# Performance work log

Measured on AMD Instinct MI355X. Metric: run time of the kernel, lower is better.

## Reference

```python
import jax, jax.numpy as jnp
import numpy as np

B, H, W, C = 8, 224, 224, 96
WS, SS, NH = 7, 3, 3  # window size, shift size, num heads
HD = C // NH
N = WS * WS
nW = (H // WS) * (W // WS)


def _rel_pos_index():
    coords = np.stack(np.meshgrid(np.arange(WS), np.arange(WS), indexing='ij'))  # (2,WS,WS)
    flat = coords.reshape(2, -1)
    rel = (flat[:, :, None] - flat[:, None, :]).transpose(1, 2, 0)  # (N,N,2)
    rel[:, :, 0] += WS - 1
    rel[:, :, 1] += WS - 1
    rel[:, :, 0] *= 2 * WS - 1
    return jnp.asarray(rel.sum(-1))  # (N,N) int


def _shift_mask():
    img = np.zeros((H, W), np.int32)
    cnt = 0
    sls = (slice(0, -WS), slice(-WS, -SS), slice(-SS, None))
    for hs in sls:
        for ws_ in sls:
            img[hs, ws_] = cnt
            cnt += 1
    m = img.reshape(H // WS, WS, W // WS, WS).transpose(0, 2, 1, 3).reshape(-1, N)  # (nW,N)
    diff = m[:, :, None] - m[:, None, :]
    return jnp.asarray(np.where(diff != 0, -100.0, 0.0).astype(np.float32))  # (nW,N,N)


def setup_inputs() -> dict:
    key = jax.random.key(0)
    ks = jax.random.split(key, 10)
    s = 0.02
    return {
        'x': jax.random.normal(ks[0], (B, H * W, C), jnp.float32),
        'mask': _shift_mask(),
        'norm1_g': jnp.ones((C,), jnp.float32),
        'norm1_b': jnp.zeros((C,), jnp.float32),
        'qkv_w': s * jax.random.normal(ks[1], (3 * C, C), jnp.float32),
        'qkv_b': jnp.zeros((3 * C,), jnp.float32),
        'rpb_table': s * jax.random.normal(ks[2], ((2 * WS - 1) * (2 * WS - 1), NH), jnp.float32),
        'proj_w': s * jax.random.normal(ks[3], (C, C), jnp.float32),
        'proj_b': jnp.zeros((C,), jnp.float32),
        'norm2_g': jnp.ones((C,), jnp.float32),
        'norm2_b': jnp.zeros((C,), jnp.float32),
        'fc1_w': s * jax.random.normal(ks[4], (4 * C, C), jnp.float32),
        'fc1_b': jnp.zeros((4 * C,), jnp.float32),
        'fc2_w': s * jax.random.normal(ks[5], (C, 4 * C), jnp.float32),
        'fc2_b': jnp.zeros((C,), jnp.float32),
    }


def _ln(x, g, b):
    mu = x.mean(-1, keepdims=True)
    var = x.var(-1, keepdims=True)
    return (x - mu) * jax.lax.rsqrt(var + 1e-5) * g + b


def _win_partition(x):  # (B,H,W,C) -> (B*nW, N, C)
    x = x.reshape(B, H // WS, WS, W // WS, WS, C)
    return x.transpose(0, 1, 3, 2, 4, 5).reshape(-1, N, C)


def _win_reverse(w):  # (B*nW, N, C) -> (B,H,W,C)
    w = w.reshape(B, H // WS, W // WS, WS, WS, C)
    return w.transpose(0, 1, 3, 2, 4, 5).reshape(B, H, W, C)


def reference(x, mask, norm1_g, norm1_b, qkv_w, qkv_b, rpb_table, proj_w, proj_b,
              norm2_g, norm2_b, fc1_w, fc1_b, fc2_w, fc2_b):
    rel_idx = _rel_pos_index()  # (N,N) constant
    shortcut = x
    h = _ln(x, norm1_g, norm1_b).reshape(B, H, W, C)
    h = jnp.roll(h, shift=(-SS, -SS), axis=(1, 2))  # cyclic shift
    xw = _win_partition(h)  # (B*nW, N, C)
    B_ = xw.shape[0]
    qkv = (xw @ qkv_w.T + qkv_b).reshape(B_, N, 3, NH, HD).transpose(2, 0, 3, 1, 4)
    q, k, v = qkv[0], qkv[1], qkv[2]  # (B_,NH,N,HD)
    scale = HD ** -0.5
    attn = jnp.einsum('bhid,bhjd->bhij', q * scale, k)  # (B_,NH,N,N)
    bias = rpb_table[rel_idx.reshape(-1)].reshape(N, N, NH).transpose(2, 0, 1)  # (NH,N,N)
    attn = attn + bias[None]
    attn = attn.reshape(B, nW, NH, N, N) + mask[None, :, None]
    attn = jax.nn.softmax(attn.reshape(B_, NH, N, N), axis=-1)
    out = jnp.einsum('bhij,bhjd->bhid', attn, v).transpose(0, 2, 1, 3).reshape(B_, N, C)
    out = out @ proj_w.T + proj_b
    h = _win_reverse(out)
    h = jnp.roll(h, shift=(SS, SS), axis=(1, 2)).reshape(B, H * W, C)
    x = shortcut + h
    # MLP
    m = _ln(x, norm2_g, norm2_b)
    m = jax.nn.gelu(m @ fc1_w.T + fc1_b, approximate=False)
    m = m @ fc2_w.T + fc2_b
    return x + m
```

## Files before the change

kernel.cpp:

```cpp
#include <hip/hip_runtime.h>
#include <hip/hip_bf16.h>
#include <stdint.h>

typedef __attribute__((ext_vector_type(4))) float f32x4;
typedef __bf16 bfv8 __attribute__((ext_vector_type(8)));
typedef unsigned short u16x8 __attribute__((ext_vector_type(8)));
typedef unsigned short u16x4 __attribute__((ext_vector_type(4)));

#define DEV static __device__ __forceinline__

DEV float b2f(unsigned short h) {
    unsigned u = ((unsigned)h) << 16;
    return __builtin_bit_cast(float, u);
}
DEV unsigned short f2b(float f) {
    unsigned u = __builtin_bit_cast(unsigned, f);
    u += 0x7fffu + ((u >> 16) & 1u);
    return (unsigned short)(u >> 16);
}
DEV unsigned short f2bn(float f) {
    return __builtin_bit_cast(unsigned short, (__bf16)f);
}
DEV bfv8 ldb8(const unsigned short* p) {
    return __builtin_bit_cast(bfv8, *(const u16x8*)p);
}
DEV void stb4(unsigned short* p, f32x4 v) {
    u16x4 o;
    o[0] = f2bn(v[0]); o[1] = f2bn(v[1]); o[2] = f2bn(v[2]); o[3] = f2bn(v[3]);
    *(u16x4*)p = o;
}

static constexpr int T = 401408;

__global__ __launch_bounds__(256) void k_prep(const float* __restrict__ qkvw,
                                              const float* __restrict__ projw,
                                              const float* __restrict__ w1,
                                              const float* __restrict__ w2,
                                              const float* __restrict__ rpb,
                                              const float* __restrict__ mask,
                                              unsigned short* __restrict__ wb,
                                              float* __restrict__ cmb) {
    int i = blockIdx.x * 256 + threadIdx.x;
    if (i < 110592) {
        float v;
        if (i < 27648) v = qkvw[i];
        else if (i < 36864) v = projw[i - 27648];
        else if (i < 73728) v = w1[i - 36864];
        else v = w2[i - 73728];
        wb[i] = f2b(v);
    } else if (i < 110592 + 49152) {
        int j = i - 110592;
        int t = j / 12288, rem = j - t * 12288;
        int h = rem >> 12, nm = rem & 4095;
        int n = nm >> 6, m = nm & 63;
        float v = -10000.f;
        if (n < 49 && m < 49) {
            int i1 = n / 7, j1 = n - i1 * 7, i2 = m / 7, j2 = m - i2 * 7;
            int rel = (i1 - i2 + 6) * 13 + (j1 - j2 + 6);
            int rep = ((t & 1) ? 31 : 0) + ((t & 2) ? 992 : 0);
            v = rpb[rel * 3 + h] + mask[rep * 2401 + n * 49 + m];
        }
        cmb[j] = v;
    }
}

__global__ __launch_bounds__(192) void k_attnf(const float* __restrict__ x,
                                               const float* __restrict__ g1,
                                               const float* __restrict__ be1,
                                               const unsigned short* __restrict__ qkvwb,
                                               const float* __restrict__ qkvb,
                                               const float* __restrict__ cmb,
                                               unsigned short* __restrict__ aout) {
    __shared__ unsigned short smem[10368 + 3 * 5120];
    unsigned short* xs = smem;

    unsigned win = blockIdx.x;
    unsigned b = win >> 10, widx = win & 1023u;
    unsigned wi = widx >> 5, wj = widx & 31u;
    int tid = threadIdx.x, wv = tid >> 6, lane = tid & 63;
    int half = lane >> 5, lch = lane & 31;

    for (int it = 0; it < 9; ++it) {
        int tok = it * 6 + wv * 2 + half;
        if (tok < 49) {
            unsigned i = (unsigned)tok / 7u, j = (unsigned)tok - i * 7u;
            unsigned sr = wi * 7 + i + 3; if (sr >= 224) sr -= 224;
            unsigned sc = wj * 7 + j + 3; if (sc >= 224) sc -= 224;
            const float* src = x + (size_t)(b * 50176u + sr * 224u + sc) * 96;
            float v0 = src[lch], v1 = src[lch + 32], v2 = src[lch + 64];
            float s = v0 + v1 + v2, q = v0 * v0 + v1 * v1 + v2 * v2;
#pragma unroll
            for (int off = 1; off < 32; off <<= 1) {
                s += __shfl_xor(s, off);
                q += __shfl_xor(q, off);
            }
            float mu = s * (1.f / 96.f);
            float rstd = rsqrtf(q * (1.f / 96.f) - mu * mu + 1e-5f);
            xs[tok * 104 + lch]      = f2bn((v0 - mu) * rstd * g1[lch] + be1[lch]);
            xs[tok * 104 + lch + 32] = f2bn((v1 - mu) * rstd * g1[lch + 32] + be1[lch + 32]);
            xs[tok * 104 + lch + 64] = f2bn((v2 - mu) * rstd * g1[lch + 64] + be1[lch + 64]);
        }
    }
    for (int t = tid; t < 15 * 96; t += 192)
        xs[(49 + t / 96) * 104 + (t % 96)] = 0;
    __syncthreads();

    int h = wv;
    int rlo = lane & 15, g4 = lane >> 4;
    bfv8 a[4][3];
#pragma unroll
    for (int mt = 0; mt < 4; ++mt)
#pragma unroll
        for (int ks = 0; ks < 3; ++ks)
            a[mt][ks] = ldb8(xs + (mt * 16 + rlo) * 104 + ks * 32 + g4 * 8);
    __syncthreads();

    unsigned short* vtH = smem + h * 3456;
    unsigned short* qH  = smem + 10368 + h * 5120;
    unsigned short* kH  = qH + 2560;
    unsigned short* pH  = qH;

    const float SC = 0.17677669529663687f;
    int colbase[6] = {32 * h, 32 * h + 16, 96 + 32 * h, 96 + 32 * h + 16,
                      192 + 32 * h, 192 + 32 * h + 16};
#pragma unroll
    for (int grp = 0; grp < 2; ++grp) {
        bfv8 wS[3][3];
        f32x4 bS[3];
#pragma unroll
        for (int q3 = 0; q3 < 3; ++q3) {
            int c = colbase[grp * 3 + q3] + rlo;
            wS[q3][0] = ldb8(qkvwb + (size_t)c * 96 + g4 * 8);
            wS[q3][1] = ldb8(qkvwb + (size_t)c * 96 + 32 + g4 * 8);
            wS[q3][2] = ldb8(qkvwb + (size_t)c * 96 + 64 + g4 * 8);
            bS[q3] = *(const f32x4*)(qkvb + colbase[grp * 3 + q3] + g4 * 4);
        }
#pragma unroll
        for (int q3 = 0; q3 < 3; ++q3) {
            int nt = grp * 3 + q3;
#pragma unroll
            for (int mt = 0; mt < 4; ++mt) {
                f32x4 acc = {0.f, 0.f, 0.f, 0.f};
                acc = __builtin_amdgcn_mfma_f32_16x16x32_bf16(wS[q3][0], a[mt][0], acc, 0, 0, 0);
                acc = __builtin_amdgcn_mfma_f32_16x16x32_bf16(wS[q3][1], a[mt][1], acc, 0, 0, 0);
                acc = __builtin_amdgcn_mfma_f32_16x16x32_bf16(wS[q3][2], a[mt][2], acc, 0, 0, 0);
                int token = mt * 16 + rlo;
                if (nt < 2) {
                    f32x4 v = (acc + bS[q3]) * SC;
                    stb4(qH + token * 40 + nt * 16 + g4 * 4, v);
                } else if (nt < 4) {
                    f32x4 v = acc + bS[q3];
                    stb4(kH + token * 40 + (nt - 2) * 16 + g4 * 4, v);
                } else {
#pragma unroll
                    for (int r = 0; r < 4; ++r)
                        vtH[((nt - 4) * 16 + g4 * 4 + r) * 72 + token] =
                            f2bn(acc[r] + bS[q3][r]);
                }
            }
        }
    }
    vtH[32 * 72 + lane] = 0x3F80;

    bfv8 qf[4], kf[4];
#pragma unroll
    for (int t = 0; t < 4; ++t) {
        qf[t] = ldb8(qH + (t * 16 + rlo) * 40 + g4 * 8);
        kf[t] = ldb8(kH + (t * 16 + rlo) * 40 + g4 * 8);
    }
    f32x4 s[4][4];
#pragma unroll
    for (int mt = 0; mt < 4; ++mt)
#pragma unroll
        for (int nt = 0; nt < 4; ++nt) {
            f32x4 acc0 = {0.f, 0.f, 0.f, 0.f};
            s[mt][nt] = __builtin_amdgcn_mfma_f32_16x16x32_bf16(kf[nt], qf[mt], acc0, 0, 0, 0);
        }
    int type = ((wi == 31) ? 2 : 0) | ((wj == 31) ? 1 : 0);
    const float* crow = cmb + ((size_t)(type * 3 + h) << 12);
#pragma unroll
    for (int mt = 0; mt < 4; ++mt) {
        int query = mt * 16 + rlo;
        const float* cr = crow + query * 64;
#pragma unroll
        for (int nt = 0; nt < 4; ++nt) {
            f32x4 cv = *(const f32x4*)(cr + nt * 16 + g4 * 4);
            f32x4 p;
#pragma unroll
            for (int r = 0; r < 4; ++r) p[r] = __expf(s[mt][nt][r] + cv[r]);
            stb4(pH + query * 72 + nt * 16 + g4 * 4, p);
        }
    }
    bfv8 vf[2][3];
#pragma unroll
    for (int ks = 0; ks < 2; ++ks)
#pragma unroll
        for (int db = 0; db < 3; ++db)
            vf[ks][db] = ldb8(vtH + (db * 16 + rlo) * 72 + ks * 32 + g4 * 8);
#pragma unroll
    for (int mt = 0; mt < 4; ++mt) {
        bfv8 pa0 = ldb8(pH + (mt * 16 + rlo) * 72 + g4 * 8);
        bfv8 pa1 = ldb8(pH + (mt * 16 + rlo) * 72 + 32 + g4 * 8);
        f32x4 acc[3];
#pragma unroll
        for (int db = 0; db < 3; ++db) {
            acc[db] = {0.f, 0.f, 0.f, 0.f};
            acc[db] = __builtin_amdgcn_mfma_f32_16x16x32_bf16(vf[0][db], pa0, acc[db], 0, 0, 0);
            acc[db] = __builtin_amdgcn_mfma_f32_16x16x32_bf16(vf[1][db], pa1, acc[db], 0, 0, 0);
        }
        float inv = 1.f / __shfl(acc[2][0], rlo);
        int query = mt * 16 + rlo;
        if (query < 49) {
            unsigned short* ob = aout + ((size_t)win * 49 + query) * 96 + h * 32;
#pragma unroll
            for (int db = 0; db < 2; ++db) {
                f32x4 v = acc[db] * inv;
                stb4(ob + db * 16 + g4 * 4, v);
            }
        }
    }
}

__global__ __launch_bounds__(256, 3) void k_pm(const unsigned short* __restrict__ aout,
                                               const unsigned short* __restrict__ projwb,
                                               const float* __restrict__ projb,
                                               const float* __restrict__ x,
                                               const float* __restrict__ g2,
                                               const float* __restrict__ be2,
                                               const unsigned short* __restrict__ w1b,
                                               const float* __restrict__ bias1,
                                               const unsigned short* __restrict__ w2b,
                                               const float* __restrict__ bias2,
                                               float* __restrict__ out) {
    __shared__ unsigned short smem[64 * 204];
    unsigned short* xn  = smem;
    unsigned short* m1t = smem;

    int lane = threadIdx.x & 63, wv = threadIdx.x >> 6;
    int rlo = lane & 15, g4 = lane >> 4;
    size_t tok0 = (size_t)blockIdx.x * 64;
    size_t rowW = tok0 + wv * 16;

    bfv8 a0[3];
    {
        const unsigned short* p = aout + (rowW + rlo) * 96 + g4 * 8;
        a0[0] = ldb8(p); a0[1] = ldb8(p + 32); a0[2] = ldb8(p + 64);
    }
    int pix;
    {
        unsigned wt = (unsigned)(rowW + rlo);
        unsigned win = wt / 49u, n = wt - win * 49u;
        unsigned b = win >> 10, widx = win & 1023u;
        unsigned wi = widx >> 5, wj = widx & 31u;
        unsigned i = n / 7u, j = n - i * 7u;
        unsigned sr = wi * 7 + i + 3; if (sr >= 224) sr -= 224;
        unsigned sc = wj * 7 + j + 3; if (sc >= 224) sc -= 224;
        pix = (int)(b * 50176u + sr * 224u + sc);
    }
    f32x4 xr4[6];
#pragma unroll
    for (int nt = 0; nt < 6; ++nt)
        xr4[nt] = *(const f32x4*)(x + (size_t)pix * 96 + nt * 16 + g4 * 4);

    f32x4 xv[6];
    float rs = 0.f, rq = 0.f;
    for (int nt = 0; nt < 6; ++nt) {
        int c = nt * 16 + rlo;
        bfv8 b0 = ldb8(projwb + (size_t)c * 96 + g4 * 8);
        bfv8 b1 = ldb8(projwb + (size_t)c * 96 + 32 + g4 * 8);
        bfv8 b2 = ldb8(projwb + (size_t)c * 96 + 64 + g4 * 8);
        f32x4 bv = *(const f32x4*)(projb + nt * 16 + g4 * 4);
        f32x4 acc = {0.f, 0.f, 0.f, 0.f};
        acc = __builtin_amdgcn_mfma_f32_16x16x32_bf16(b0, a0[0], acc, 0, 0, 0);
        acc = __builtin_amdgcn_mfma_f32_16x16x32_bf16(b1, a0[1], acc, 0, 0, 0);
        acc = __builtin_amdgcn_mfma_f32_16x16x32_bf16(b2, a0[2], acc, 0, 0, 0);
        f32x4 v = acc + bv + xr4[nt];
        xv[nt] = v;
#pragma unroll
        for (int r = 0; r < 4; ++r) {
            rs += v[r];
            rq += v[r] * v[r];
        }
    }
    rs += __shfl_xor(rs, 16); rq += __shfl_xor(rq, 16);
    rs += __shfl_xor(rs, 32); rq += __shfl_xor(rq, 32);
    float mu = rs * (1.f / 96.f);
    float rstd = rsqrtf(rq * (1.f / 96.f) - mu * mu + 1e-5f);
#pragma unroll
    for (int nt = 0; nt < 6; ++nt) {
        f32x4 gg = *(const f32x4*)(g2 + nt * 16 + g4 * 4);
        f32x4 bb = *(const f32x4*)(be2 + nt * 16 + g4 * 4);
        f32x4 v;
#pragma unroll
        for (int r = 0; r < 4; ++r) v[r] = (xv[nt][r] - mu) * rstd * gg[r] + bb[r];
        stb4(xn + (wv * 16 + rlo) * 104 + nt * 16 + g4 * 4, v);
    }
    __syncthreads();

    bfv8 a[4][3];
#pragma unroll
    for (int mt = 0; mt < 4; ++mt)
#pragma unroll
        for (int ks = 0; ks < 3; ++ks)
            a[mt][ks] = ldb8(xn + (mt * 16 + rlo) * 104 + ks * 32 + g4 * 8);
    __syncthreads();

    f32x4 acc2[6];
#pragma unroll
    for (int nt = 0; nt < 6; ++nt) acc2[nt] = {0.f, 0.f, 0.f, 0.f};

#pragma unroll
    for (int half = 0; half < 2; ++half) {
#pragma unroll
        for (int nt = 0; nt < 3; ++nt) {
            int cb = half * 192 + wv * 48 + nt * 16;
            int c = cb + rlo;
            bfv8 b0 = ldb8(w1b + (size_t)c * 96 + g4 * 8);
            bfv8 b1 = ldb8(w1b + (size_t)c * 96 + 32 + g4 * 8);
            bfv8 b2 = ldb8(w1b + (size_t)c * 96 + 64 + g4 * 8);
            f32x4 bv = *(const f32x4*)(bias1 + cb + g4 * 4);
#pragma unroll
            for (int mt = 0; mt < 4; ++mt) {
                f32x4 acc = {0.f, 0.f, 0.f, 0.f};
                acc = __builtin_amdgcn_mfma_f32_16x16x32_bf16(b0, a[mt][0], acc, 0, 0, 0);
                acc = __builtin_amdgcn_mfma_f32_16x16x32_bf16(b1, a[mt][1], acc, 0, 0, 0);
                acc = __builtin_amdgcn_mfma_f32_16x16x32_bf16(b2, a[mt][2], acc, 0, 0, 0);
                f32x4 g;
#pragma unroll
                for (int r = 0; r < 4; ++r) {
                    float v = acc[r] + bv[r];
                    float z = 1.5957691216057308f * (v + 0.044715f * v * v * v);
                    g[r] = v / (1.f + __expf(-z));
                }
                stb4(m1t + (mt * 16 + rlo) * 204 + wv * 48 + nt * 16 + g4 * 4, g);
            }
        }
        __syncthreads();
#pragma unroll
        for (int ks = 0; ks < 6; ++ks) {
            bfv8 am = ldb8(m1t + (wv * 16 + rlo) * 204 + ks * 32 + g4 * 8);
#pragma unroll
            for (int nt = 0; nt < 6; ++nt) {
                bfv8 bw = ldb8(w2b + (size_t)(nt * 16 + rlo) * 384 + half * 192 + ks * 32 + g4 * 8);
                acc2[nt] = __builtin_amdgcn_mfma_f32_16x16x32_bf16(bw, am, acc2[nt], 0, 0, 0);
            }
        }
        if (half == 0) __syncthreads();
    }

#pragma unroll
    for (int nt = 0; nt < 6; ++nt) {
        f32x4 bv = *(const f32x4*)(bias2 + nt * 16 + g4 * 4);
        f32x4 ov = acc2[nt] + bv + xv[nt];
        *(f32x4*)(out + (size_t)pix * 96 + nt * 16 + g4 * 4) = ov;
    }
}

extern "C" void kernel_launch(void* const* d_in, const int* in_sizes, int n_in,
                              void* d_out, int out_size, void* d_ws, size_t ws_size,
                              hipStream_t stream) {
    const float* x     = (const float*)d_in[0];
    const float* mask  = (const float*)d_in[1];
    const float* n1g   = (const float*)d_in[2];
    const float* n1b   = (const float*)d_in[3];
    const float* qkvw  = (const float*)d_in[4];
    const float* qkvb  = (const float*)d_in[5];
    const float* rpb   = (const float*)d_in[6];
    const float* projw = (const float*)d_in[7];
    const float* projb = (const float*)d_in[8];
    const float* n2g   = (const float*)d_in[9];
    const float* n2b   = (const float*)d_in[10];
    const float* fc1w  = (const float*)d_in[11];
    const float* fc1b  = (const float*)d_in[12];
    const float* fc2w  = (const float*)d_in[13];
    const float* fc2b  = (const float*)d_in[14];

    if (ws_size < 77488128ULL) return;
    char* ws = (char*)d_ws;
    unsigned short* aout = (unsigned short*)ws;
    unsigned short* wb   = (unsigned short*)(ws + 77070336);
    float*          cmb  = (float*)(ws + 77291520);
    float*          out  = (float*)d_out;

    unsigned short* qkvwb  = wb;
    unsigned short* projwb = wb + 27648;
    unsigned short* fc1wb  = wb + 36864;
    unsigned short* fc2wb  = wb + 73728;

    k_prep<<<624, 256, 0, stream>>>(qkvw, projw, fc1w, fc2w, rpb, mask, wb, cmb);
    k_attnf<<<8192, 192, 0, stream>>>(x, n1g, n1b, qkvwb, qkvb, cmb, aout);
    k_pm<<<T / 64, 256, 0, stream>>>(aout, projwb, projb, x, n2g, n2b,
                                     fc1wb, fc1b, fc2wb, fc2b, out);
}
```

Baseline: 520.4 us.

## Rewrite MLP kernel as single-wave tiles using register shuffles instead of LDS

The proj+MLP kernel changes from 4-wave blocks of 64 tokens sharing LDS to 1-wave blocks of 16 tokens. The LayerNorm output and the GELU hidden activations are moved from the MFMA accumulator layout into the operand layout with cross-lane shuffles, so no shared memory and no __syncthreads are needed. The cost is that each wave now loads the full fc1/fc2 weights for only 16 tokens instead of sharing them across 64, which quadruples weight traffic through L1/L2. It also adds shuffle instructions in the inner loop.

```diff
diff --git a/kernel.cpp b/kernel.cpp
--- a/kernel.cpp
+++ b/kernel.cpp
@@ -6,6 +6,7 @@
 typedef __bf16 bfv8 __attribute__((ext_vector_type(8)));
 typedef unsigned short u16x8 __attribute__((ext_vector_type(8)));
 typedef unsigned short u16x4 __attribute__((ext_vector_type(4)));
+typedef unsigned int u32x4 __attribute__((ext_vector_type(4)));
 
 #define DEV static __device__ __forceinline__
 
@@ -28,6 +29,25 @@
     u16x4 o;
     o[0] = f2bn(v[0]); o[1] = f2bn(v[1]); o[2] = f2bn(v[2]); o[3] = f2bn(v[3]);
     *(u16x4*)p = o;
+}
+DEV uint2 pk4(f32x4 v) {
+    uint2 r;
+    r.x = (unsigned)f2bn(v[0]) | ((unsigned)f2bn(v[1]) << 16);
+    r.y = (unsigned)f2bn(v[2]) | ((unsigned)f2bn(v[3]) << 16);
+    return r;
+}
+DEV bfv8 permfrag(uint2 e, uint2 o, int s0, bool sel) {
+    int s1 = s0 + 16;
+    unsigned e0 = __shfl((int)e.x, s0), o0 = __shfl((int)o.x, s0);
+    unsigned e1 = __shfl((int)e.y, s0), o1 = __shfl((int)o.y, s0);
+    unsigned e2 = __shfl((int)e.x, s1), o2 = __shfl((int)o.x, s1);
+    unsigned e3 = __shfl((int)e.y, s1), o3 = __shfl((int)o.y, s1);
+    u32x4 u;
+    u[0] = sel ? o0 : e0;
+    u[1] = sel ? o1 : e1;
+    u[2] = sel ? o2 : e2;
+    u[3] = sel ? o3 : e3;
+    return __builtin_bit_cast(bfv8, u);
 }
 
 static constexpr int T = 401408;
@@ -221,25 +241,20 @@
     }
 }
 
-__global__ __launch_bounds__(256, 3) void k_pm(const unsigned short* __restrict__ aout,
-                                               const unsigned short* __restrict__ projwb,
-                                               const float* __restrict__ projb,
-                                               const float* __restrict__ x,
-                                               const float* __restrict__ g2,
-                                               const float* __restrict__ be2,
-                                               const unsigned short* __restrict__ w1b,
-                                               const float* __restrict__ bias1,
-                                               const unsigned short* __restrict__ w2b,
-                                               const float* __restrict__ bias2,
-                                               float* __restrict__ out) {
-    __shared__ unsigned short smem[64 * 204];
-    unsigned short* xn  = smem;
-    unsigned short* m1t = smem;
-
-    int lane = threadIdx.x & 63, wv = threadIdx.x >> 6;
+__global__ __launch_bounds__(64, 3) void k_pm(const unsigned short* __restrict__ aout,
+                                              const unsigned short* __restrict__ projwb,
+                                              const float* __restrict__ projb,
+                                              const float* __restrict__ x,
+                                              const float* __restrict__ g2,
+                                              const float* __restrict__ be2,
+                                              const unsigned short* __restrict__ w1b,
+                                              const float* __restrict__ bias1,
+                                              const unsigned short* __restrict__ w2b,
+                                              const float* __restrict__ bias2,
+                                              float* __restrict__ out) {
+    int lane = threadIdx.x & 63;
     int rlo = lane & 15, g4 = lane >> 4;
-    size_t tok0 = (size_t)blockIdx.x * 64;
-    size_t rowW = tok0 + wv * 16;
+    size_t rowW = (size_t)blockIdx.x * 16;
 
     bfv8 a0[3];
     {
@@ -264,6 +279,7 @@
 
     f32x4 xv[6];
     float rs = 0.f, rq = 0.f;
+#pragma unroll
     for (int nt = 0; nt < 6; ++nt) {
         int c = nt * 16 + rlo;
         bfv8 b0 = ldb8(projwb + (size_t)c * 96 + g4 * 8);
@@ -286,6 +302,8 @@
     rs += __shfl_xor(rs, 32); rq += __shfl_xor(rq, 32);
     float mu = rs * (1.f / 96.f);
     float rstd = rsqrtf(rq * (1.f / 96.f) - mu * mu + 1e-5f);
+
+    uint2 ln[6];
 #pragma unroll
     for (int nt = 0; nt < 6; ++nt) {
         f32x4 gg = *(const f32x4*)(g2 + nt * 16 + g4 * 4);
@@ -293,59 +311,47 @@
         f32x4 v;
 #pragma unroll
         for (int r = 0; r < 4; ++r) v[r] = (xv[nt][r] - mu) * rstd * gg[r] + bb[r];
-        stb4(xn + (wv * 16 + rlo) * 104 + nt * 16 + g4 * 4, v);
-    }
-    __syncthreads();
-
-    bfv8 a[4][3];
-#pragma unroll
-    for (int mt = 0; mt < 4; ++mt)
-#pragma unroll
-        for (int ks = 0; ks < 3; ++ks)
-            a[mt][ks] = ldb8(xn + (mt * 16 + rlo) * 104 + ks * 32 + g4 * 8);
-    __syncthreads();
+        ln[nt] = pk4(v);
+    }
+    int s0 = rlo + ((g4 & 1) << 5);
+    bool sel = (g4 >> 1) != 0;
+    bfv8 fb[3];
+#pragma unroll
+    for (int kin = 0; kin < 3; ++kin)
+        fb[kin] = permfrag(ln[2 * kin], ln[2 * kin + 1], s0, sel);
 
     f32x4 acc2[6];
 #pragma unroll
     for (int nt = 0; nt < 6; ++nt) acc2[nt] = {0.f, 0.f, 0.f, 0.f};
-
-#pragma unroll
-    for (int half = 0; half < 2; ++half) {
-#pragma unroll
-        for (int nt = 0; nt < 3; ++nt) {
-            int cb = half * 192 + wv * 48 + nt * 16;
-            int c = cb + rlo;
-            bfv8 b0 = ldb8(w1b + (size_t)c * 96 + g4 * 8);
-            bfv8 b1 = ldb8(w1b + (size_t)c * 96 + 32 + g4 * 8);
-            bfv8 b2 = ldb8(w1b + (size_t)c * 96 + 64 + g4 * 8);
-            f32x4 bv = *(const f32x4*)(bias1 + cb + g4 * 4);
-#pragma unroll
-            for (int mt = 0; mt < 4; ++mt) {
-                f32x4 acc = {0.f, 0.f, 0.f, 0.f};
-                acc = __builtin_amdgcn_mfma_f32_16x16x32_bf16(b0, a[mt][0], acc, 0, 0, 0);
-                acc = __builtin_amdgcn_mfma_f32_16x16x32_bf16(b1, a[mt][1], acc, 0, 0, 0);
-                acc = __builtin_amdgcn_mfma_f32_16x16x32_bf16(b2, a[mt][2], acc, 0, 0, 0);
-                f32x4 g;
-#pragma unroll
-                for (int r = 0; r < 4; ++r) {
-                    float v = acc[r] + bv[r];
-                    float z = 1.5957691216057308f * (v + 0.044715f * v * v * v);
-                    g[r] = v / (1.f + __expf(-z));
-                }
-                stb4(m1t + (mt * 16 + rlo) * 204 + wv * 48 + nt * 16 + g4 * 4, g);
+    for (int ks = 0; ks < 12; ++ks) {
+        uint2 g1p[2];
+#pragma unroll
+        for (int t = 0; t < 2; ++t) {
+            int ct = (ks * 2 + t) * 16;
+            int c = ct + rlo;
+            bfv8 w0 = ldb8(w1b + (size_t)c * 96 + g4 * 8);
+            bfv8 w1_ = ldb8(w1b + (size_t)c * 96 + 32 + g4 * 8);
+            bfv8 w2_ = ldb8(w1b + (size_t)c * 96 + 64 + g4 * 8);
+            f32x4 bv = *(const f32x4*)(bias1 + ct + g4 * 4);
+            f32x4 acc = {0.f, 0.f, 0.f, 0.f};
+            acc = __builtin_amdgcn_mfma_f32_16x16x32_bf16(w0, fb[0], acc, 0, 0, 0);
+            acc = __builtin_amdgcn_mfma_f32_16x16x32_bf16(w1_, fb[1], acc, 0, 0, 0);
+            acc = __builtin_amdgcn_mfma_f32_16x16x32_bf16(w2_, fb[2], acc, 0, 0, 0);
+            f32x4 g;
+#pragma unroll
+            for (int r = 0; r < 4; ++r) {
+                float v = acc[r] + bv[r];
+                float z = 1.5957691216057308f * (v + 0.044715f * v * v * v);
+                g[r] = v / (1.f + __expf(-z));
             }
-        }
-        __syncthreads();
-#pragma unroll
-        for (int ks = 0; ks < 6; ++ks) {
-            bfv8 am = ldb8(m1t + (wv * 16 + rlo) * 204 + ks * 32 + g4 * 8);
-#pragma unroll
-            for (int nt = 0; nt < 6; ++nt) {
-                bfv8 bw = ldb8(w2b + (size_t)(nt * 16 + rlo) * 384 + half * 192 + ks * 32 + g4 * 8);
-                acc2[nt] = __builtin_amdgcn_mfma_f32_16x16x32_bf16(bw, am, acc2[nt], 0, 0, 0);
-            }
-        }
-        if (half == 0) __syncthreads();
+            g1p[t] = pk4(g);
+        }
+        bfv8 mf = permfrag(g1p[0], g1p[1], s0, sel);
+#pragma unroll
+        for (int nt = 0; nt < 6; ++nt) {
+            bfv8 bw = ldb8(w2b + (size_t)(nt * 16 + rlo) * 384 + ks * 32 + g4 * 8);
+            acc2[nt] = __builtin_amdgcn_mfma_f32_16x16x32_bf16(bw, mf, acc2[nt], 0, 0, 0);
+        }
     }
 
 #pragma unroll
@@ -389,6 +395,6 @@
 
     k_prep<<<624, 256, 0, stream>>>(qkvw, projw, fc1w, fc2w, rpb, mask, wb, cmb);
     k_attnf<<<8192, 192, 0, stream>>>(x, n1g, n1b, qkvwb, qkvb, cmb, aout);
-    k_pm<<<T / 64, 256, 0, stream>>>(aout, projwb, projb, x, n2g, n2b,
-                                     fc1wb, fc1b, fc2wb, fc2b, out);
-}
+    k_pm<<<T / 16, 64, 0, stream>>>(aout, projwb, projb, x, n2g, n2b,
+                                    fc1wb, fc1b, fc2wb, fc2b, out);
+}
```

Measured after the change: 605.5 us. 1.16x slower.

## Fuse window attention with projection and MLP into one per-window kernel

Applied to the files above, without the earlier changes.

Merges the attention kernel and the proj+LN2+MLP kernel into a single kernel with one 256-thread block per window. The attention output stays in shared memory instead of round-tripping through a bf16 global buffer. The 4th wave idles during attention, and the MLP now runs on 64 padded rows for 49 real tokens, so about 23% of the MLP tensor-core work is wasted. Shared memory per block grows, which may reduce occupancy.

```diff
diff --git a/kernel.cpp b/kernel.cpp
--- a/kernel.cpp
+++ b/kernel.cpp
@@ -64,24 +64,36 @@
     }
 }
 
-__global__ __launch_bounds__(192) void k_attnf(const float* __restrict__ x,
-                                               const float* __restrict__ g1,
-                                               const float* __restrict__ be1,
-                                               const unsigned short* __restrict__ qkvwb,
-                                               const float* __restrict__ qkvb,
-                                               const float* __restrict__ cmb,
-                                               unsigned short* __restrict__ aout) {
-    __shared__ unsigned short smem[10368 + 3 * 5120];
-    unsigned short* xs = smem;
+__global__ __launch_bounds__(256, 3) void k_fused(const float* __restrict__ x,
+                                                  const float* __restrict__ g1,
+                                                  const float* __restrict__ be1,
+                                                  const unsigned short* __restrict__ qkvwb,
+                                                  const float* __restrict__ qkvb,
+                                                  const float* __restrict__ cmb,
+                                                  const unsigned short* __restrict__ projwb,
+                                                  const float* __restrict__ projb,
+                                                  const float* __restrict__ g2,
+                                                  const float* __restrict__ be2,
+                                                  const unsigned short* __restrict__ w1b,
+                                                  const float* __restrict__ bias1,
+                                                  const unsigned short* __restrict__ w2b,
+                                                  const float* __restrict__ bias2,
+                                                  float* __restrict__ out) {
+    __shared__ unsigned short smem[25728];
+    unsigned short* xs  = smem;
+    unsigned short* at  = smem;
+    unsigned short* xn  = smem + 13312;
+    unsigned short* m1t = smem;
 
     unsigned win = blockIdx.x;
     unsigned b = win >> 10, widx = win & 1023u;
     unsigned wi = widx >> 5, wj = widx & 31u;
     int tid = threadIdx.x, wv = tid >> 6, lane = tid & 63;
     int half = lane >> 5, lch = lane & 31;
-
-    for (int it = 0; it < 9; ++it) {
-        int tok = it * 6 + wv * 2 + half;
+    int rlo = lane & 15, g4 = lane >> 4;
+
+    for (int it = 0; it < 7; ++it) {
+        int tok = it * 8 + wv * 2 + half;
         if (tok < 49) {
             unsigned i = (unsigned)tok / 7u, j = (unsigned)tok - i * 7u;
             unsigned sr = wi * 7 + i + 3; if (sr >= 224) sr -= 224;
@@ -101,18 +113,19 @@
             xs[tok * 104 + lch + 64] = f2bn((v2 - mu) * rstd * g1[lch + 64] + be1[lch + 64]);
         }
     }
-    for (int t = tid; t < 15 * 96; t += 192)
+    for (int t = tid; t < 15 * 96; t += 256)
         xs[(49 + t / 96) * 104 + (t % 96)] = 0;
     __syncthreads();
 
     int h = wv;
-    int rlo = lane & 15, g4 = lane >> 4;
     bfv8 a[4][3];
-#pragma unroll
-    for (int mt = 0; mt < 4; ++mt)
-#pragma unroll
-        for (int ks = 0; ks < 3; ++ks)
-            a[mt][ks] = ldb8(xs + (mt * 16 + rlo) * 104 + ks * 32 + g4 * 8);
+    if (wv < 3) {
+#pragma unroll
+        for (int mt = 0; mt < 4; ++mt)
+#pragma unroll
+            for (int ks = 0; ks < 3; ++ks)
+                a[mt][ks] = ldb8(xs + (mt * 16 + rlo) * 104 + ks * 32 + g4 * 8);
+    }
     __syncthreads();
 
     unsigned short* vtH = smem + h * 3456;
@@ -120,139 +133,125 @@
     unsigned short* kH  = qH + 2560;
     unsigned short* pH  = qH;
 
-    const float SC = 0.17677669529663687f;
-    int colbase[6] = {32 * h, 32 * h + 16, 96 + 32 * h, 96 + 32 * h + 16,
-                      192 + 32 * h, 192 + 32 * h + 16};
-#pragma unroll
-    for (int grp = 0; grp < 2; ++grp) {
-        bfv8 wS[3][3];
-        f32x4 bS[3];
-#pragma unroll
-        for (int q3 = 0; q3 < 3; ++q3) {
-            int c = colbase[grp * 3 + q3] + rlo;
-            wS[q3][0] = ldb8(qkvwb + (size_t)c * 96 + g4 * 8);
-            wS[q3][1] = ldb8(qkvwb + (size_t)c * 96 + 32 + g4 * 8);
-            wS[q3][2] = ldb8(qkvwb + (size_t)c * 96 + 64 + g4 * 8);
-            bS[q3] = *(const f32x4*)(qkvb + colbase[grp * 3 + q3] + g4 * 4);
-        }
-#pragma unroll
-        for (int q3 = 0; q3 < 3; ++q3) {
-            int nt = grp * 3 + q3;
-#pragma unroll
-            for (int mt = 0; mt < 4; ++mt) {
-                f32x4 acc = {0.f, 0.f, 0.f, 0.f};
-                acc = __builtin_amdgcn_mfma_f32_16x16x32_bf16(wS[q3][0], a[mt][0], acc, 0, 0, 0);
-                acc = __builtin_amdgcn_mfma_f32_16x16x32_bf16(wS[q3][1], a[mt][1], acc, 0, 0, 0);
-                acc = __builtin_amdgcn_mfma_f32_16x16x32_bf16(wS[q3][2], a[mt][2], acc, 0, 0, 0);
-                int token = mt * 16 + rlo;
-                if (nt < 2) {
-                    f32x4 v = (acc + bS[q3]) * SC;
-                    stb4(qH + token * 40 + nt * 16 + g4 * 4, v);
-                } else if (nt < 4) {
-                    f32x4 v = acc + bS[q3];
-                    stb4(kH + token * 40 + (nt - 2) * 16 + g4 * 4, v);
-                } else {
-#pragma unroll
-                    for (int r = 0; r < 4; ++r)
-                        vtH[((nt - 4) * 16 + g4 * 4 + r) * 72 + token] =
-                            f2bn(acc[r] + bS[q3][r]);
+    bfv8 vf[2][3];
+    if (wv < 3) {
+        const float SC = 0.17677669529663687f;
+        int colbase[6] = {32 * h, 32 * h + 16, 96 + 32 * h, 96 + 32 * h + 16,
+                          192 + 32 * h, 192 + 32 * h + 16};
+#pragma unroll
+        for (int grp = 0; grp < 2; ++grp) {
+            bfv8 wS[3][3];
+            f32x4 bS[3];
+#pragma unroll
+            for (int q3 = 0; q3 < 3; ++q3) {
+                int c = colbase[grp * 3 + q3] + rlo;
+                wS[q3][0] = ldb8(qkvwb + (size_t)c * 96 + g4 * 8);
+                wS[q3][1] = ldb8(qkvwb + (size_t)c * 96 + 32 + g4 * 8);
+                wS[q3][2] = ldb8(qkvwb + (size_t)c * 96 + 64 + g4 * 8);
+                bS[q3] = *(const f32x4*)(qkvb + colbase[grp * 3 + q3] + g4 * 4);
+            }
+#pragma unroll
+            for (int q3 = 0; q3 < 3; ++q3) {
+                int nt = grp * 3 + q3;
+#pragma unroll
+                for (int mt = 0; mt < 4; ++mt) {
+                    f32x4 acc = {0.f, 0.f, 0.f, 0.f};
+                    acc = __builtin_amdgcn_mfma_f32_16x16x32_bf16(wS[q3][0], a[mt][0], acc, 0, 0, 0);
+                    acc = __builtin_amdgcn_mfma_f32_16x16x32_bf16(wS[q3][1], a[mt][1], acc, 0, 0, 0);
+                    acc = __builtin_amdgcn_mfma_f32_16x16x32_bf16(wS[q3][2], a[mt][2], acc, 0, 0, 0);
+                    int token = mt * 16 + rlo;
+                    if (nt < 2) {
+                        f32x4 v = (acc + bS[q3]) * SC;
+                        stb4(qH + token * 40 + nt * 16 + g4 * 4, v);
+                    } else if (nt < 4) {
+                        f32x4 v = acc + bS[q3];
+                        stb4(kH + token * 40 + (nt - 2) * 16 + g4 * 4, v);
+                    } else {
+#pragma unroll
+                        for (int r = 0; r < 4; ++r)
+                            vtH[((nt - 4) * 16 + g4 * 4 + r) * 72 + token] =
+                                f2bn(acc[r] + bS[q3][r]);
+                    }
                 }
             }
         }
-    }
-    vtH[32 * 72 + lane] = 0x3F80;
-
-    bfv8 qf[4], kf[4];
-#pragma unroll
-    for (int t = 0; t < 4; ++t) {
-        qf[t] = ldb8(qH + (t * 16 + rlo) * 40 + g4 * 8);
-        kf[t] = ldb8(kH + (t * 16 + rlo) * 40 + g4 * 8);
-    }
+        vtH[32 * 72 + lane] = 0x3F80;
+    }
+
     f32x4 s[4][4];
-#pragma unroll
-    for (int mt = 0; mt < 4; ++mt)
-#pragma unroll
-        for (int nt = 0; nt < 4; ++nt) {
-            f32x4 acc0 = {0.f, 0.f, 0.f, 0.f};
-            s[mt][nt] = __builtin_amdgcn_mfma_f32_16x16x32_bf16(kf[nt], qf[mt], acc0, 0, 0, 0);
-        }
-    int type = ((wi == 31) ? 2 : 0) | ((wj == 31) ? 1 : 0);
-    const float* crow = cmb + ((size_t)(type * 3 + h) << 12);
-#pragma unroll
-    for (int mt = 0; mt < 4; ++mt) {
-        int query = mt * 16 + rlo;
-        const float* cr = crow + query * 64;
-#pragma unroll
-        for (int nt = 0; nt < 4; ++nt) {
-            f32x4 cv = *(const f32x4*)(cr + nt * 16 + g4 * 4);
-            f32x4 p;
-#pragma unroll
-            for (int r = 0; r < 4; ++r) p[r] = __expf(s[mt][nt][r] + cv[r]);
-            stb4(pH + query * 72 + nt * 16 + g4 * 4, p);
-        }
-    }
-    bfv8 vf[2][3];
-#pragma unroll
-    for (int ks = 0; ks < 2; ++ks)
-#pragma unroll
-        for (int db = 0; db < 3; ++db)
-            vf[ks][db] = ldb8(vtH + (db * 16 + rlo) * 72 + ks * 32 + g4 * 8);
-#pragma unroll
-    for (int mt = 0; mt < 4; ++mt) {
-        bfv8 pa0 = ldb8(pH + (mt * 16 + rlo) * 72 + g4 * 8);
-        bfv8 pa1 = ldb8(pH + (mt * 16 + rlo) * 72 + 32 + g4 * 8);
-        f32x4 acc[3];
-#pragma unroll
-        for (int db = 0; db < 3; ++db) {
-            acc[db] = {0.f, 0.f, 0.f, 0.f};
-            acc[db] = __builtin_amdgcn_mfma_f32_16x16x32_bf16(vf[0][db], pa0, acc[db], 0, 0, 0);
-            acc[db] = __builtin_amdgcn_mfma_f32_16x16x32_bf16(vf[1][db], pa1, acc[db], 0, 0, 0);
-        }
-        float inv = 1.f / __shfl(acc[2][0], rlo);
-        int query = mt * 16 + rlo;
-        if (query < 49) {
-            unsigned short* ob = aout + ((size_t)win * 49 + query) * 96 + h * 32;
-#pragma unroll
-            for (int db = 0; db < 2; ++db) {
-                f32x4 v = acc[db] * inv;
-                stb4(ob + db * 16 + g4 * 4, v);
-            }
-        }
-    }
-}
-
-__global__ __launch_bounds__(256, 3) void k_pm(const unsigned short* __restrict__ aout,
-                                               const unsigned short* __restrict__ projwb,
-                                               const float* __restrict__ projb,
-                                               const float* __restrict__ x,
-                                               const float* __restrict__ g2,
-                                               const float* __restrict__ be2,
-                                               const unsigned short* __restrict__ w1b,
-                                               const float* __restrict__ bias1,
-                                               const unsigned short* __restrict__ w2b,
-                                               const float* __restrict__ bias2,
-                                               float* __restrict__ out) {
-    __shared__ unsigned short smem[64 * 204];
-    unsigned short* xn  = smem;
-    unsigned short* m1t = smem;
-
-    int lane = threadIdx.x & 63, wv = threadIdx.x >> 6;
-    int rlo = lane & 15, g4 = lane >> 4;
-    size_t tok0 = (size_t)blockIdx.x * 64;
-    size_t rowW = tok0 + wv * 16;
-
+    if (wv < 3) {
+        bfv8 qf[4], kf[4];
+#pragma unroll
+        for (int t = 0; t < 4; ++t) {
+            qf[t] = ldb8(qH + (t * 16 + rlo) * 40 + g4 * 8);
+            kf[t] = ldb8(kH + (t * 16 + rlo) * 40 + g4 * 8);
+        }
+#pragma unroll
+        for (int mt = 0; mt < 4; ++mt)
+#pragma unroll
+            for (int nt = 0; nt < 4; ++nt) {
+                f32x4 acc0 = {0.f, 0.f, 0.f, 0.f};
+                s[mt][nt] = __builtin_amdgcn_mfma_f32_16x16x32_bf16(kf[nt], qf[mt], acc0, 0, 0, 0);
+            }
+        int type = ((wi == 31) ? 2 : 0) | ((wj == 31) ? 1 : 0);
+        const float* crow = cmb + ((size_t)(type * 3 + h) << 12);
+#pragma unroll
+        for (int mt = 0; mt < 4; ++mt) {
+            int query = mt * 16 + rlo;
+            const float* cr = crow + query * 64;
+#pragma unroll
+            for (int nt = 0; nt < 4; ++nt) {
+                f32x4 cv = *(const f32x4*)(cr + nt * 16 + g4 * 4);
+                f32x4 p;
+#pragma unroll
+                for (int r = 0; r < 4; ++r) p[r] = __expf(s[mt][nt][r] + cv[r]);
+                stb4(pH + query * 72 + nt * 16 + g4 * 4, p);
+            }
+        }
+#pragma unroll
+        for (int ks = 0; ks < 2; ++ks)
+#pragma unroll
+            for (int db = 0; db < 3; ++db)
+                vf[ks][db] = ldb8(vtH + (db * 16 + rlo) * 72 + ks * 32 + g4 * 8);
+    }
+    __syncthreads();
+
+    if (wv < 3) {
+#pragma unroll
+        for (int mt = 0; mt < 4; ++mt) {
+            bfv8 pa0 = ldb8(pH + (mt * 16 + rlo) * 72 + g4 * 8);
+            bfv8 pa1 = ldb8(pH + (mt * 16 + rlo) * 72 + 32 + g4 * 8);
+            f32x4 acc[3];
+#pragma unroll
+            for (int db = 0; db < 3; ++db) {
+                acc[db] = {0.f, 0.f, 0.f, 0.f};
+                acc[db] = __builtin_amdgcn_mfma_f32_16x16x32_bf16(vf[0][db], pa0, acc[db], 0, 0, 0);
+                acc[db] = __builtin_amdgcn_mfma_f32_16x16x32_bf16(vf[1][db], pa1, acc[db], 0, 0, 0);
+            }
+            float inv = 1.f / __shfl(acc[2][0], rlo);
+            int query = mt * 16 + rlo;
+            if (query < 49) {
+#pragma unroll
+                for (int db = 0; db < 2; ++db) {
+                    f32x4 v = acc[db] * inv;
+                    stb4(at + query * 104 + h * 32 + db * 16 + g4 * 4, v);
+                }
+            }
+        }
+    }
+    for (int t = tid; t < 15 * 104; t += 256)
+        at[(49 + t / 104) * 104 + (t % 104)] = 0;
+    __syncthreads();
+
+    int n = wv * 16 + rlo;
     bfv8 a0[3];
     {
-        const unsigned short* p = aout + (rowW + rlo) * 96 + g4 * 8;
+        const unsigned short* p = at + n * 104 + g4 * 8;
         a0[0] = ldb8(p); a0[1] = ldb8(p + 32); a0[2] = ldb8(p + 64);
     }
     int pix;
     {
-        unsigned wt = (unsigned)(rowW + rlo);
-        unsigned win = wt / 49u, n = wt - win * 49u;
-        unsigned b = win >> 10, widx = win & 1023u;
-        unsigned wi = widx >> 5, wj = widx & 31u;
-        unsigned i = n / 7u, j = n - i * 7u;
+        unsigned i = (unsigned)n / 7u, j = (unsigned)n - i * 7u;
         unsigned sr = wi * 7 + i + 3; if (sr >= 224) sr -= 224;
         unsigned sc = wj * 7 + j + 3; if (sc >= 224) sc -= 224;
         pix = (int)(b * 50176u + sr * 224u + sc);
@@ -264,6 +263,7 @@
 
     f32x4 xv[6];
     float rs = 0.f, rq = 0.f;
+#pragma unroll
     for (int nt = 0; nt < 6; ++nt) {
         int c = nt * 16 + rlo;
         bfv8 b0 = ldb8(projwb + (size_t)c * 96 + g4 * 8);
@@ -293,16 +293,16 @@
         f32x4 v;
 #pragma unroll
         for (int r = 0; r < 4; ++r) v[r] = (xv[nt][r] - mu) * rstd * gg[r] + bb[r];
-        stb4(xn + (wv * 16 + rlo) * 104 + nt * 16 + g4 * 4, v);
-    }
-    __syncthreads();
-
-    bfv8 a[4][3];
+        stb4(xn + n * 104 + nt * 16 + g4 * 4, v);
+    }
+    __syncthreads();
+
+    bfv8 af[4][3];
 #pragma unroll
     for (int mt = 0; mt < 4; ++mt)
 #pragma unroll
         for (int ks = 0; ks < 3; ++ks)
-            a[mt][ks] = ldb8(xn + (mt * 16 + rlo) * 104 + ks * 32 + g4 * 8);
+            af[mt][ks] = ldb8(xn + (mt * 16 + rlo) * 104 + ks * 32 + g4 * 8);
     __syncthreads();
 
     f32x4 acc2[6];
@@ -310,10 +310,10 @@
     for (int nt = 0; nt < 6; ++nt) acc2[nt] = {0.f, 0.f, 0.f, 0.f};
 
 #pragma unroll
-    for (int half = 0; half < 2; ++half) {
+    for (int hf = 0; hf < 2; ++hf) {
 #pragma unroll
         for (int nt = 0; nt < 3; ++nt) {
-            int cb = half * 192 + wv * 48 + nt * 16;
+            int cb = hf * 192 + wv * 48 + nt * 16;
             int c = cb + rlo;
             bfv8 b0 = ldb8(w1b + (size_t)c * 96 + g4 * 8);
             bfv8 b1 = ldb8(w1b + (size_t)c * 96 + 32 + g4 * 8);
@@ -322,9 +322,9 @@
 #pragma unroll
             for (int mt = 0; mt < 4; ++mt) {
                 f32x4 acc = {0.f, 0.f, 0.f, 0.f};
-                acc = __builtin_amdgcn_mfma_f32_16x16x32_bf16(b0, a[mt][0], acc, 0, 0, 0);
-                acc = __builtin_amdgcn_mfma_f32_16x16x32_bf16(b1, a[mt][1], acc, 0, 0, 0);
-                acc = __builtin_amdgcn_mfma_f32_16x16x32_bf16(b2, a[mt][2], acc, 0, 0, 0);
+                acc = __builtin_amdgcn_mfma_f32_16x16x32_bf16(b0, af[mt][0], acc, 0, 0, 0);
+                acc = __builtin_amdgcn_mfma_f32_16x16x32_bf16(b1, af[mt][1], acc, 0, 0, 0);
+                acc = __builtin_amdgcn_mfma_f32_16x16x32_bf16(b2, af[mt][2], acc, 0, 0, 0);
                 f32x4 g;
 #pragma unroll
                 for (int r = 0; r < 4; ++r) {
@@ -341,18 +341,20 @@
             bfv8 am = ldb8(m1t + (wv * 16 + rlo) * 204 + ks * 32 + g4 * 8);
 #pragma unroll
             for (int nt = 0; nt < 6; ++nt) {
-                bfv8 bw = ldb8(w2b + (size_t)(nt * 16 + rlo) * 384 + half * 192 + ks * 32 + g4 * 8);
+                bfv8 bw = ldb8(w2b + (size_t)(nt * 16 + rlo) * 384 + hf * 192 + ks * 32 + g4 * 8);
                 acc2[nt] = __builtin_amdgcn_mfma_f32_16x16x32_bf16(bw, am, acc2[nt], 0, 0, 0);
             }
         }
-        if (half == 0) __syncthreads();
-    }
-
-#pragma unroll
-    for (int nt = 0; nt < 6; ++nt) {
-        f32x4 bv = *(const f32x4*)(bias2 + nt * 16 + g4 * 4);
-        f32x4 ov = acc2[nt] + bv + xv[nt];
-        *(f32x4*)(out + (size_t)pix * 96 + nt * 16 + g4 * 4) = ov;
+        if (hf == 0) __syncthreads();
+    }
+
+    if (n < 49) {
+#pragma unroll
+        for (int nt = 0; nt < 6; ++nt) {
+            f32x4 bv = *(const f32x4*)(bias2 + nt * 16 + g4 * 4);
+            f32x4 ov = acc2[nt] + bv + xv[nt];
+            *(f32x4*)(out + (size_t)pix * 96 + nt * 16 + g4 * 4) = ov;
+        }
     }
 }
 
@@ -375,12 +377,11 @@
     const float* fc2w  = (const float*)d_in[13];
     const float* fc2b  = (const float*)d_in[14];
 
-    if (ws_size < 77488128ULL) return;
+    if (ws_size < 417792ULL) return;
     char* ws = (char*)d_ws;
-    unsigned short* aout = (unsigned short*)ws;
-    unsigned short* wb   = (unsigned short*)(ws + 77070336);
-    float*          cmb  = (float*)(ws + 77291520);
-    float*          out  = (float*)d_out;
+    unsigned short* wb  = (unsigned short*)ws;
+    float*          cmb = (float*)(ws + 221184);
+    float*          out = (float*)d_out;
 
     unsigned short* qkvwb  = wb;
     unsigned short* projwb = wb + 27648;
@@ -388,7 +389,7 @@
     unsigned short* fc2wb  = wb + 73728;
 
     k_prep<<<624, 256, 0, stream>>>(qkvw, projw, fc1w, fc2w, rpb, mask, wb, cmb);
-    k_attnf<<<8192, 192, 0, stream>>>(x, n1g, n1b, qkvwb, qkvb, cmb, aout);
-    k_pm<<<T / 64, 256, 0, stream>>>(aout, projwb, projb, x, n2g, n2b,
-                                     fc1wb, fc1b, fc2wb, fc2b, out);
-}
+    k_fused<<<8192, 256, 0, stream>>>(x, n1g, n1b, qkvwb, qkvb, cmb,
+                                      projwb, projb, n2g, n2b,
+                                      fc1wb, fc1b, fc2wb, fc2b, out);
+}
```

Result: slower. 553.4 us (+6.3%).

## Halve k_pm block to two waves, each handling two 16-row tiles

Applied to the files above, without the earlier changes.

Shrinks the fused proj+LN+MLP kernel from four to two waves per block, with each wave now processing two 16-token row tiles. Each weight fragment loaded from global memory is reused across twice as many MFMAs, which cuts weight load traffic per token. To relieve register pressure, the intermediate residual is written to the output buffer and read back for the final add instead of being kept live. The cost is more VGPRs per wave, fewer waves to hide latency, and an extra global round trip for the residual.

```diff
diff --git a/kernel.cpp b/kernel.cpp
--- a/kernel.cpp
+++ b/kernel.cpp
@@ -221,7 +221,7 @@
     }
 }
 
-__global__ __launch_bounds__(256, 3) void k_pm(const unsigned short* __restrict__ aout,
+__global__ __launch_bounds__(128, 3) void k_pm(const unsigned short* __restrict__ aout,
                                                const unsigned short* __restrict__ projwb,
                                                const float* __restrict__ projb,
                                                const float* __restrict__ x,
@@ -239,81 +239,86 @@
     int lane = threadIdx.x & 63, wv = threadIdx.x >> 6;
     int rlo = lane & 15, g4 = lane >> 4;
     size_t tok0 = (size_t)blockIdx.x * 64;
-    size_t rowW = tok0 + wv * 16;
-
-    bfv8 a0[3];
-    {
-        const unsigned short* p = aout + (rowW + rlo) * 96 + g4 * 8;
-        a0[0] = ldb8(p); a0[1] = ldb8(p + 32); a0[2] = ldb8(p + 64);
-    }
-    int pix;
-    {
-        unsigned wt = (unsigned)(rowW + rlo);
+
+    bfv8 a0[2][3];
+    int pix[2];
+#pragma unroll
+    for (int t = 0; t < 2; ++t) {
+        int tt = 2 * wv + t;
+        const unsigned short* p = aout + (tok0 + tt * 16 + rlo) * 96 + g4 * 8;
+        a0[t][0] = ldb8(p); a0[t][1] = ldb8(p + 32); a0[t][2] = ldb8(p + 64);
+        unsigned wt = (unsigned)(tok0 + tt * 16 + rlo);
         unsigned win = wt / 49u, n = wt - win * 49u;
         unsigned b = win >> 10, widx = win & 1023u;
         unsigned wi = widx >> 5, wj = widx & 31u;
         unsigned i = n / 7u, j = n - i * 7u;
         unsigned sr = wi * 7 + i + 3; if (sr >= 224) sr -= 224;
         unsigned sc = wj * 7 + j + 3; if (sc >= 224) sc -= 224;
-        pix = (int)(b * 50176u + sr * 224u + sc);
-    }
-    f32x4 xr4[6];
-#pragma unroll
-    for (int nt = 0; nt < 6; ++nt)
-        xr4[nt] = *(const f32x4*)(x + (size_t)pix * 96 + nt * 16 + g4 * 4);
-
-    f32x4 xv[6];
-    float rs = 0.f, rq = 0.f;
+        pix[t] = (int)(b * 50176u + sr * 224u + sc);
+    }
+
+    f32x4 xv[2][6];
+    float rs[2] = {0.f, 0.f}, rq[2] = {0.f, 0.f};
+#pragma unroll
     for (int nt = 0; nt < 6; ++nt) {
         int c = nt * 16 + rlo;
         bfv8 b0 = ldb8(projwb + (size_t)c * 96 + g4 * 8);
         bfv8 b1 = ldb8(projwb + (size_t)c * 96 + 32 + g4 * 8);
         bfv8 b2 = ldb8(projwb + (size_t)c * 96 + 64 + g4 * 8);
         f32x4 bv = *(const f32x4*)(projb + nt * 16 + g4 * 4);
-        f32x4 acc = {0.f, 0.f, 0.f, 0.f};
-        acc = __builtin_amdgcn_mfma_f32_16x16x32_bf16(b0, a0[0], acc, 0, 0, 0);
-        acc = __builtin_amdgcn_mfma_f32_16x16x32_bf16(b1, a0[1], acc, 0, 0, 0);
-        acc = __builtin_amdgcn_mfma_f32_16x16x32_bf16(b2, a0[2], acc, 0, 0, 0);
-        f32x4 v = acc + bv + xr4[nt];
-        xv[nt] = v;
-#pragma unroll
-        for (int r = 0; r < 4; ++r) {
-            rs += v[r];
-            rq += v[r] * v[r];
-        }
-    }
-    rs += __shfl_xor(rs, 16); rq += __shfl_xor(rq, 16);
-    rs += __shfl_xor(rs, 32); rq += __shfl_xor(rq, 32);
-    float mu = rs * (1.f / 96.f);
-    float rstd = rsqrtf(rq * (1.f / 96.f) - mu * mu + 1e-5f);
-#pragma unroll
-    for (int nt = 0; nt < 6; ++nt) {
-        f32x4 gg = *(const f32x4*)(g2 + nt * 16 + g4 * 4);
-        f32x4 bb = *(const f32x4*)(be2 + nt * 16 + g4 * 4);
-        f32x4 v;
-#pragma unroll
-        for (int r = 0; r < 4; ++r) v[r] = (xv[nt][r] - mu) * rstd * gg[r] + bb[r];
-        stb4(xn + (wv * 16 + rlo) * 104 + nt * 16 + g4 * 4, v);
+#pragma unroll
+        for (int t = 0; t < 2; ++t) {
+            f32x4 acc = {0.f, 0.f, 0.f, 0.f};
+            acc = __builtin_amdgcn_mfma_f32_16x16x32_bf16(b0, a0[t][0], acc, 0, 0, 0);
+            acc = __builtin_amdgcn_mfma_f32_16x16x32_bf16(b1, a0[t][1], acc, 0, 0, 0);
+            acc = __builtin_amdgcn_mfma_f32_16x16x32_bf16(b2, a0[t][2], acc, 0, 0, 0);
+            f32x4 xr = *(const f32x4*)(x + (size_t)pix[t] * 96 + nt * 16 + g4 * 4);
+            f32x4 v = acc + bv + xr;
+            xv[t][nt] = v;
+            *(f32x4*)(out + (size_t)pix[t] * 96 + nt * 16 + g4 * 4) = v;
+            rs[t] += v[0] + v[1] + v[2] + v[3];
+            rq[t] += v[0] * v[0] + v[1] * v[1] + v[2] * v[2] + v[3] * v[3];
+        }
+    }
+#pragma unroll
+    for (int t = 0; t < 2; ++t) {
+        float s = rs[t], q = rq[t];
+        s += __shfl_xor(s, 16); q += __shfl_xor(q, 16);
+        s += __shfl_xor(s, 32); q += __shfl_xor(q, 32);
+        float mu = s * (1.f / 96.f);
+        float rstd = rsqrtf(q * (1.f / 96.f) - mu * mu + 1e-5f);
+        int row = (2 * wv + t) * 16 + rlo;
+#pragma unroll
+        for (int nt = 0; nt < 6; ++nt) {
+            f32x4 gg = *(const f32x4*)(g2 + nt * 16 + g4 * 4);
+            f32x4 bb = *(const f32x4*)(be2 + nt * 16 + g4 * 4);
+            f32x4 v;
+#pragma unroll
+            for (int r = 0; r < 4; ++r) v[r] = (xv[t][nt][r] - mu) * rstd * gg[r] + bb[r];
+            stb4(xn + row * 104 + nt * 16 + g4 * 4, v);
+        }
     }
     __syncthreads();
 
-    bfv8 a[4][3];
+    bfv8 af[4][3];
 #pragma unroll
     for (int mt = 0; mt < 4; ++mt)
 #pragma unroll
         for (int ks = 0; ks < 3; ++ks)
-            a[mt][ks] = ldb8(xn + (mt * 16 + rlo) * 104 + ks * 32 + g4 * 8);
+            af[mt][ks] = ldb8(xn + (mt * 16 + rlo) * 104 + ks * 32 + g4 * 8);
     __syncthreads();
 
-    f32x4 acc2[6];
-#pragma unroll
-    for (int nt = 0; nt < 6; ++nt) acc2[nt] = {0.f, 0.f, 0.f, 0.f};
+    f32x4 acc2[2][6];
+#pragma unroll
+    for (int t = 0; t < 2; ++t)
+#pragma unroll
+        for (int nt = 0; nt < 6; ++nt) acc2[t][nt] = {0.f, 0.f, 0.f, 0.f};
 
 #pragma unroll
     for (int half = 0; half < 2; ++half) {
 #pragma unroll
-        for (int nt = 0; nt < 3; ++nt) {
-            int cb = half * 192 + wv * 48 + nt * 16;
+        for (int nt = 0; nt < 6; ++nt) {
+            int cb = half * 192 + wv * 96 + nt * 16;
             int c = cb + rlo;
             bfv8 b0 = ldb8(w1b + (size_t)c * 96 + g4 * 8);
             bfv8 b1 = ldb8(w1b + (size_t)c * 96 + 32 + g4 * 8);
@@ -322,9 +327,9 @@
 #pragma unroll
             for (int mt = 0; mt < 4; ++mt) {
                 f32x4 acc = {0.f, 0.f, 0.f, 0.f};
-                acc = __builtin_amdgcn_mfma_f32_16x16x32_bf16(b0, a[mt][0], acc, 0, 0, 0);
-                acc = __builtin_amdgcn_mfma_f32_16x16x32_bf16(b1, a[mt][1], acc, 0, 0, 0);
-                acc = __builtin_amdgcn_mfma_f32_16x16x32_bf16(b2, a[mt][2], acc, 0, 0, 0);
+                acc = __builtin_amdgcn_mfma_f32_16x16x32_bf16(b0, af[mt][0], acc, 0, 0, 0);
+                acc = __builtin_amdgcn_mfma_f32_16x16x32_bf16(b1, af[mt][1], acc, 0, 0, 0);
+                acc = __builtin_amdgcn_mfma_f32_16x16x32_bf16(b2, af[mt][2], acc, 0, 0, 0);
                 f32x4 g;
 #pragma unroll
                 for (int r = 0; r < 4; ++r) {
@@ -332,28 +337,33 @@
                     float z = 1.5957691216057308f * (v + 0.044715f * v * v * v);
                     g[r] = v / (1.f + __expf(-z));
                 }
-                stb4(m1t + (mt * 16 + rlo) * 204 + wv * 48 + nt * 16 + g4 * 4, g);
+                stb4(m1t + (mt * 16 + rlo) * 204 + wv * 96 + nt * 16 + g4 * 4, g);
             }
         }
         __syncthreads();
 #pragma unroll
         for (int ks = 0; ks < 6; ++ks) {
-            bfv8 am = ldb8(m1t + (wv * 16 + rlo) * 204 + ks * 32 + g4 * 8);
+            bfv8 am0 = ldb8(m1t + ((2 * wv + 0) * 16 + rlo) * 204 + ks * 32 + g4 * 8);
+            bfv8 am1 = ldb8(m1t + ((2 * wv + 1) * 16 + rlo) * 204 + ks * 32 + g4 * 8);
 #pragma unroll
             for (int nt = 0; nt < 6; ++nt) {
                 bfv8 bw = ldb8(w2b + (size_t)(nt * 16 + rlo) * 384 + half * 192 + ks * 32 + g4 * 8);
-                acc2[nt] = __builtin_amdgcn_mfma_f32_16x16x32_bf16(bw, am, acc2[nt], 0, 0, 0);
+                acc2[0][nt] = __builtin_amdgcn_mfma_f32_16x16x32_bf16(bw, am0, acc2[0][nt], 0, 0, 0);
+                acc2[1][nt] = __builtin_amdgcn_mfma_f32_16x16x32_bf16(bw, am1, acc2[1][nt], 0, 0, 0);
             }
         }
         if (half == 0) __syncthreads();
     }
 
 #pragma unroll
-    for (int nt = 0; nt < 6; ++nt) {
-        f32x4 bv = *(const f32x4*)(bias2 + nt * 16 + g4 * 4);
-        f32x4 ov = acc2[nt] + bv + xv[nt];
-        *(f32x4*)(out + (size_t)pix * 96 + nt * 16 + g4 * 4) = ov;
-    }
+    for (int t = 0; t < 2; ++t)
+#pragma unroll
+        for (int nt = 0; nt < 6; ++nt) {
+            f32x4 bv = *(const f32x4*)(bias2 + nt * 16 + g4 * 4);
+            f32x4 x1v = *(const f32x4*)(out + (size_t)pix[t] * 96 + nt * 16 + g4 * 4);
+            f32x4 ov = acc2[t][nt] + bv + x1v;
+            *(f32x4*)(out + (size_t)pix[t] * 96 + nt * 16 + g4 * 4) = ov;
+        }
 }
 
 extern "C" void kernel_launch(void* const* d_in, const int* in_sizes, int n_in,
@@ -389,6 +399,6 @@
 
     k_prep<<<624, 256, 0, stream>>>(qkvw, projw, fc1w, fc2w, rpb, mask, wb, cmb);
     k_attnf<<<8192, 192, 0, stream>>>(x, n1g, n1b, qkvwb, qkvb, cmb, aout);
-    k_pm<<<T / 64, 256, 0, stream>>>(aout, projwb, projb, x, n2g, n2b,
+    k_pm<<<T / 64, 128, 0, stream>>>(aout, projwb, projb, x, n2g, n2b,
                                      fc1wb, fc1b, fc2wb, fc2b, out);
 }
```

Result: faster. 494.7 us (-4.9%).
